# Kernel optimization log

Measured on AMD Instinct MI355X. Metric: run time of the kernel, lower is better.

Reference implementation:

```python
import jax, jax.numpy as jnp
import numpy as np

INPUT_SIZE = 4
HIDDEN = 2048
OUTPUT_SIZE = 2
NOISE_STD = 0.05
ALPHA = 0.2
RANK = 2
N_SUPPORTS = 2
GDIM = 2 * RANK + INPUT_SIZE  # gaussian_basis_dim default
BATCH = 32
SEQ = 1000


def setup_inputs() -> dict:
    key = jax.random.key(0)
    ks = jax.random.split(key, 8)
    inp = jax.random.normal(ks[0], (BATCH, SEQ, INPUT_SIZE), dtype=jnp.float32)
    noise = jax.random.normal(ks[1], (BATCH, SEQ, HIDDEN), dtype=jnp.float32)
    gaussian_basis = jax.random.normal(ks[2], (GDIM, HIDDEN), dtype=jnp.float32)
    # supports: block indicator masks over hidden units (equal split, weights=None)
    sup = np.zeros((N_SUPPORTS, HIDDEN), dtype=np.float32)
    l = HIDDEN // N_SUPPORTS
    for i in range(N_SUPPORTS):
        sup[i, l * i:l * (i + 1)] = 1.0
    supports = jnp.asarray(sup)
    wi_weights = jax.random.normal(ks[3], (INPUT_SIZE, N_SUPPORTS, GDIM), dtype=jnp.float32)
    m_weights = jax.random.normal(ks[4], (RANK, N_SUPPORTS, GDIM), dtype=jnp.float32) / jnp.sqrt(jnp.float32(HIDDEN))
    n_weights = jax.random.normal(ks[5], (RANK, N_SUPPORTS, GDIM), dtype=jnp.float32) / jnp.sqrt(jnp.float32(HIDDEN))
    wo_weights = jax.random.normal(ks[6], (OUTPUT_SIZE, N_SUPPORTS, GDIM), dtype=jnp.float32) / jnp.float32(HIDDEN)
    wi_biases = jnp.zeros((INPUT_SIZE, N_SUPPORTS), dtype=jnp.float32)
    m_biases = jnp.zeros((RANK, N_SUPPORTS), dtype=jnp.float32)
    n_biases = jnp.zeros((RANK, N_SUPPORTS), dtype=jnp.float32)
    h0_weights = jnp.zeros((N_SUPPORTS, GDIM), dtype=jnp.float32)
    return {
        "input": inp, "noise": noise,
        "wi_weights": wi_weights, "m_weights": m_weights, "n_weights": n_weights,
        "wo_weights": wo_weights, "wi_biases": wi_biases, "m_biases": m_biases,
        "n_biases": n_biases, "h0_weights": h0_weights,
        "gaussian_basis": gaussian_basis, "supports": supports,
    }


def _proxy_params(wi_weights, m_weights, n_weights, wo_weights,
                  wi_biases, m_biases, n_biases, h0_weights,
                  gaussian_basis, supports):
    # (X, S, G) @ (G, H) -> (X, S, H); mask by supports (S, H); sum over S
    def mix(w):
        return jnp.einsum('xsg,gh->xsh', w, gaussian_basis)
    wi = jnp.sum(mix(wi_weights) * supports, axis=1) + wi_biases @ supports      # (I, H)
    m = (jnp.sum(mix(m_weights) * supports, axis=1) + m_biases @ supports).T     # (H, R)
    n = (jnp.sum(mix(n_weights) * supports, axis=1) + n_biases @ supports).T     # (H, R)
    wo = jnp.sum(mix(wo_weights) * supports, axis=1).T                            # (H, O)
    h0 = jnp.sum((h0_weights @ gaussian_basis) * supports, axis=0)                # (H,)
    return wi, m, n, wo, h0


def reference(input, noise, wi_weights, m_weights, n_weights, wo_weights,
              wi_biases, m_biases, n_biases, h0_weights, gaussian_basis, supports):
    wi, m, n, wo, h0 = _proxy_params(wi_weights, m_weights, n_weights, wo_weights,
                                     wi_biases, m_biases, n_biases, h0_weights,
                                     gaussian_basis, supports)
    B = input.shape[0]
    # Precompute external input projection for all steps: (B, T, H)
    xin = jnp.einsum('bti,ih->bth', input, wi)
    h_init = jnp.broadcast_to(h0, (B, h0.shape[0]))
    r_init = jnp.tanh(h_init)

    noise_T = jnp.swapaxes(noise, 0, 1)  # (T, B, H)
    xin_T = jnp.swapaxes(xin, 0, 1)      # (T, B, H)

    def step(carry, xs):
        h, r = carry
        noise_t, xin_t = xs
        h = h + NOISE_STD * noise_t + ALPHA * (-h + (r @ n) @ m.T + xin_t)
        r = jnp.tanh(h)
        return (h, r), r

    _, rs = jax.lax.scan(step, (h_init, r_init), (noise_T, xin_T))  # rs: (T, B, H)
    output = jnp.einsum('tbh,ho->bto', rs, wo)  # (B, T, O)
    return output
```

## Files before the change

kernel.cpp:

```cpp
#include <hip/hip_runtime.h>

#define BATCH 32
#define SEQT 1000
#define INSZ 4
#define HID 2048
#define NOISE_STD 0.05f
#define ALPHA 0.2f
#define ONE_M_ALPHA (1.0f - ALPHA)

#define NTHREADS 512
#define NWAVES 8
#define EPT 4
#define PF 4

typedef float v2f __attribute__((ext_vector_type(2)));

__device__ __forceinline__ v2f vfma(v2f a, v2f b, v2f c) { return a * b + c; }

template<int CTRL>
__device__ __forceinline__ float dpp_add(float x) {
    int s = __builtin_amdgcn_update_dpp(0, __float_as_int(x), CTRL, 0xF, 0xF, true);
    return x + __int_as_float(s);
}

__device__ __forceinline__ float wave_sum64_to_lane63(float x) {
    x = dpp_add<0x111>(x);
    x = dpp_add<0x112>(x);
    x = dpp_add<0x114>(x);
    x = dpp_add<0x118>(x);
    x = dpp_add<0x142>(x);
    x = dpp_add<0x143>(x);
    return x;
}

__device__ __forceinline__ float sum8_to_lane7(float x) {
    x = dpp_add<0x111>(x);
    x = dpp_add<0x112>(x);
    x = dpp_add<0x114>(x);
    return x;
}

__device__ __forceinline__ float read_lane7(float x) {
    return __int_as_float(__builtin_amdgcn_readlane(__float_as_int(x), 7));
}

__device__ __forceinline__ float fast_tanh(float x) {
    float e = __expf(2.0f * x);
    return 1.0f - 2.0f * __builtin_amdgcn_rcpf(e + 1.0f);
}

#define LDS_BARRIER() __asm__ volatile("s_waitcnt lgkmcnt(0)\ns_barrier" ::: "memory")

__global__ __launch_bounds__(NTHREADS)
void rnn_kernel(const float* __restrict__ input,
                const float* __restrict__ noise,
                const float* __restrict__ wi_w,
                const float* __restrict__ m_w,
                const float* __restrict__ n_w,
                const float* __restrict__ wo_w,
                const float* __restrict__ wi_b,
                const float* __restrict__ m_b,
                const float* __restrict__ n_b,
                const float* __restrict__ h0_w,
                const float* __restrict__ gb,
                const float* __restrict__ sup,
                float* __restrict__ out)
{
    __shared__ float4 sIn4[SEQT];
    __shared__ __align__(16) float4 sRed[2][NWAVES];

    const int b    = blockIdx.x;
    const int tid  = threadIdx.x;
    const int wave = tid >> 6;
    const int lane = tid & 63;

    const float4* inRow4 = reinterpret_cast<const float4*>(input + (size_t)b * SEQT * INSZ);
    for (int i = tid; i < SEQT; i += NTHREADS)
        sIn4[i] = inRow4[i];

    v2f wiA[INSZ][2];
    v2f mA0v[2], mA1v[2], n0v[2], n1v[2], wo0v[2], wo1v[2], hv[2];
    v2f q0 = {0.f, 0.f}, q1 = q0, q2 = q0, q3 = q0;

    #pragma unroll
    for (int e = 0; e < EPT; ++e) {
        const int h = tid * 4 + e;
        const int pi = e >> 1, pc = e & 1;
        float gv[8];
        #pragma unroll
        for (int g = 0; g < 8; ++g) gv[g] = gb[g * HID + h];
        const float s0 = sup[h];
        const float s1 = sup[HID + h];

        auto mix = [&](const float* w) -> float {
            float a0 = 0.f, a1 = 0.f;
            #pragma unroll
            for (int g = 0; g < 8; ++g) { a0 += w[g] * gv[g]; a1 += w[8 + g] * gv[g]; }
            return s0 * a0 + s1 * a1;
        };

        #pragma unroll
        for (int i = 0; i < INSZ; ++i)
            wiA[i][pi][pc] = ALPHA * (mix(wi_w + i * 16) + wi_b[i * 2 + 0] * s0 + wi_b[i * 2 + 1] * s1);
        mA0v[pi][pc] = ALPHA * (mix(m_w)      + m_b[0] * s0 + m_b[1] * s1);
        mA1v[pi][pc] = ALPHA * (mix(m_w + 16) + m_b[2] * s0 + m_b[3] * s1);
        const float n0 = mix(n_w)      + n_b[0] * s0 + n_b[1] * s1;
        const float n1 = mix(n_w + 16) + n_b[2] * s0 + n_b[3] * s1;
        const float w0 = mix(wo_w);
        const float w1 = mix(wo_w + 16);
        n0v[pi][pc] = n0;  n1v[pi][pc] = n1;
        wo0v[pi][pc] = w0; wo1v[pi][pc] = w1;
        {
            float a0 = 0.f, a1 = 0.f;
            #pragma unroll
            for (int g = 0; g < 8; ++g) { a0 += h0_w[g] * gv[g]; a1 += h0_w[8 + g] * gv[g]; }
            const float h0v = s0 * a0 + s1 * a1;
            hv[pi][pc] = h0v;
            const float r = fast_tanh(h0v);
            q0[pc] += r * n0;  q1[pc] += r * n1;
            q2[pc] += r * w0;  q3[pc] += r * w1;
        }
    }

    const float4* nP4 = reinterpret_cast<const float4*>(noise + (size_t)b * SEQT * HID);
    const int rowStride = HID / 4;
    float4 nb0 = nP4[0 * rowStride + tid];
    float4 nb1 = nP4[1 * rowStride + tid];
    float4 nb2 = nP4[2 * rowStride + tid];
    float4 nb3 = nP4[3 * rowStride + tid];

    float* outRow = out + (size_t)b * SEQT * 2;

    __syncthreads();
    float4 inv0 = sIn4[0];
    float4 inv1 = sIn4[1];
    float4 inv2 = sIn4[2];
    float4 inv3 = sIn4[3];

    auto do_step = [&](int t, float4& nbuf, float4& invReg) {
        const int par = t & 1;
        const float p0 = q0.x + q0.y, p1 = q1.x + q1.y;
        const float p2 = q2.x + q2.y, p3 = q3.x + q3.y;
        const float w0 = wave_sum64_to_lane63(p0);
        const float w1 = wave_sum64_to_lane63(p1);
        const float w2 = wave_sum64_to_lane63(p2);
        const float w3 = wave_sum64_to_lane63(p3);
        if (lane == 63) sRed[par][wave] = make_float4(w0, w1, w2, w3);

        LDS_BARRIER();

        const float4 pr = sRed[par][lane & 7];
        const int tpre = (t + PF < SEQT) ? (t + PF) : (SEQT - 1);
        const float4 nv4 = nbuf;
        nbuf = nP4[(size_t)tpre * rowStride + tid];
        const float4 inv = invReg;
        invReg = sIn4[tpre];

        const v2f nlo = {nv4.x, nv4.y}, nhi = {nv4.z, nv4.w};
        v2f acc0 = wiA[0][0] * inv.x;
        v2f acc1 = wiA[0][1] * inv.x;
        acc0 = vfma(wiA[1][0], inv.y, acc0);  acc1 = vfma(wiA[1][1], inv.y, acc1);
        acc0 = vfma(wiA[2][0], inv.z, acc0);  acc1 = vfma(wiA[2][1], inv.z, acc1);
        acc0 = vfma(wiA[3][0], inv.w, acc0);  acc1 = vfma(wiA[3][1], inv.w, acc1);
        acc0 = acc0 + nlo * NOISE_STD;        acc1 = acc1 + nhi * NOISE_STD;
        acc0 = vfma(hv[0], ONE_M_ALPHA, acc0); acc1 = vfma(hv[1], ONE_M_ALPHA, acc1);

        const float y0 = read_lane7(sum8_to_lane7(pr.x));
        const float y1 = read_lane7(sum8_to_lane7(pr.y));

        if (t > 0 && wave == (t & 7)) {
            const float oz = sum8_to_lane7(pr.z);
            const float ow = sum8_to_lane7(pr.w);
            if (lane == 7)
                *reinterpret_cast<float2*>(outRow + (t - 1) * 2) = make_float2(oz, ow);
        }

        v2f h2a = vfma(mA1v[0], y1, acc0);
        v2f h2b = vfma(mA1v[1], y1, acc1);
        h2a = vfma(mA0v[0], y0, h2a);
        h2b = vfma(mA0v[1], y0, h2b);
        hv[0] = h2a; hv[1] = h2b;
        v2f r2a, r2b;
        r2a.x = fast_tanh(h2a.x); r2a.y = fast_tanh(h2a.y);
        r2b.x = fast_tanh(h2b.x); r2b.y = fast_tanh(h2b.y);
        q0 = r2a * n0v[0];  q0 = vfma(r2b, n0v[1], q0);
        q1 = r2a * n1v[0];  q1 = vfma(r2b, n1v[1], q1);
        q2 = r2a * wo0v[0]; q2 = vfma(r2b, wo0v[1], q2);
        q3 = r2a * wo1v[0]; q3 = vfma(r2b, wo1v[1], q3);
    };

    for (int t = 0; t < SEQT; t += PF) {
        do_step(t,     nb0, inv0);
        do_step(t + 1, nb1, inv1);
        do_step(t + 2, nb2, inv2);
        do_step(t + 3, nb3, inv3);
    }

    {
        const float p2 = q2.x + q2.y, p3 = q3.x + q3.y;
        const float w2 = wave_sum64_to_lane63(p2);
        const float w3 = wave_sum64_to_lane63(p3);
        if (lane == 63) sRed[0][wave] = make_float4(w2, w3, 0.f, 0.f);
        LDS_BARRIER();
        if (wave == 0) {
            const float4 pr = sRed[0][lane & 7];
            const float oz = sum8_to_lane7(pr.x);
            const float ow = sum8_to_lane7(pr.y);
            if (lane == 7)
                *reinterpret_cast<float2*>(outRow + (SEQT - 1) * 2) = make_float2(oz, ow);
        }
    }
}

extern "C" void kernel_launch(void* const* d_in, const int* in_sizes, int n_in,
                              void* d_out, int out_size, void* d_ws, size_t ws_size,
                              hipStream_t stream) {
    const float* input = (const float*)d_in[0];
    const float* noise = (const float*)d_in[1];
    const float* wi_w  = (const float*)d_in[2];
    const float* m_w   = (const float*)d_in[3];
    const float* n_w   = (const float*)d_in[4];
    const float* wo_w  = (const float*)d_in[5];
    const float* wi_b  = (const float*)d_in[6];
    const float* m_b   = (const float*)d_in[7];
    const float* n_b   = (const float*)d_in[8];
    const float* h0_w  = (const float*)d_in[9];
    const float* gb    = (const float*)d_in[10];
    const float* sup   = (const float*)d_in[11];
    float* out = (float*)d_out;

    rnn_kernel<<<dim3(BATCH), dim3(NTHREADS), 0, stream>>>(
        input, noise, wi_w, m_w, n_w, wo_w, wi_b, m_b, n_b, h0_w, gb, sup, out);
}
```

Measured before the change: 877.4 us.

## Defer output wave-reductions past barrier and load input directly from global

After: 940.8 us. 7.2% more time.

```diff
diff --git a/kernel.cpp b/kernel.cpp
--- a/kernel.cpp
+++ b/kernel.cpp
@@ -66,17 +66,12 @@
                 const float* __restrict__ sup,
                 float* __restrict__ out)
 {
-    __shared__ float4 sIn4[SEQT];
     __shared__ __align__(16) float4 sRed[2][NWAVES];
 
     const int b    = blockIdx.x;
     const int tid  = threadIdx.x;
     const int wave = tid >> 6;
     const int lane = tid & 63;
-
-    const float4* inRow4 = reinterpret_cast<const float4*>(input + (size_t)b * SEQT * INSZ);
-    for (int i = tid; i < SEQT; i += NTHREADS)
-        sIn4[i] = inRow4[i];
 
     v2f wiA[INSZ][2];
     v2f mA0v[2], mA1v[2], n0v[2], n1v[2], wo0v[2], wo1v[2], hv[2];
@@ -129,32 +124,36 @@
     float4 nb2 = nP4[2 * rowStride + tid];
     float4 nb3 = nP4[3 * rowStride + tid];
 
+    const float4* inRow4 = reinterpret_cast<const float4*>(input + (size_t)b * SEQT * INSZ);
+    float4 inv0 = inRow4[0];
+    float4 inv1 = inRow4[1];
+    float4 inv2 = inRow4[2];
+    float4 inv3 = inRow4[3];
+
     float* outRow = out + (size_t)b * SEQT * 2;
 
-    __syncthreads();
-    float4 inv0 = sIn4[0];
-    float4 inv1 = sIn4[1];
-    float4 inv2 = sIn4[2];
-    float4 inv3 = sIn4[3];
+    float oz = 0.f, ow = 0.f;
 
     auto do_step = [&](int t, float4& nbuf, float4& invReg) {
         const int par = t & 1;
         const float p0 = q0.x + q0.y, p1 = q1.x + q1.y;
-        const float p2 = q2.x + q2.y, p3 = q3.x + q3.y;
         const float w0 = wave_sum64_to_lane63(p0);
         const float w1 = wave_sum64_to_lane63(p1);
-        const float w2 = wave_sum64_to_lane63(p2);
-        const float w3 = wave_sum64_to_lane63(p3);
-        if (lane == 63) sRed[par][wave] = make_float4(w0, w1, w2, w3);
+        if (lane == 63) sRed[par][wave] = make_float4(w0, w1, oz, ow);
 
         LDS_BARRIER();
 
         const float4 pr = sRed[par][lane & 7];
+
+        const float p2 = q2.x + q2.y, p3 = q3.x + q3.y;
+        const float ozn = wave_sum64_to_lane63(p2);
+        const float own = wave_sum64_to_lane63(p3);
+
         const int tpre = (t + PF < SEQT) ? (t + PF) : (SEQT - 1);
         const float4 nv4 = nbuf;
         nbuf = nP4[(size_t)tpre * rowStride + tid];
         const float4 inv = invReg;
-        invReg = sIn4[tpre];
+        invReg = inRow4[tpre];
 
         const v2f nlo = {nv4.x, nv4.y}, nhi = {nv4.z, nv4.w};
         v2f acc0 = wiA[0][0] * inv.x;
@@ -168,12 +167,13 @@
         const float y0 = read_lane7(sum8_to_lane7(pr.x));
         const float y1 = read_lane7(sum8_to_lane7(pr.y));
 
-        if (t > 0 && wave == (t & 7)) {
-            const float oz = sum8_to_lane7(pr.z);
-            const float ow = sum8_to_lane7(pr.w);
+        if (t >= 2 && wave == (t & 7)) {
+            const float o0 = sum8_to_lane7(pr.z);
+            const float o1 = sum8_to_lane7(pr.w);
             if (lane == 7)
-                *reinterpret_cast<float2*>(outRow + (t - 1) * 2) = make_float2(oz, ow);
+                *reinterpret_cast<float2*>(outRow + (t - 2) * 2) = make_float2(o0, o1);
         }
+        oz = ozn; ow = own;
 
         v2f h2a = vfma(mA1v[0], y1, acc0);
         v2f h2b = vfma(mA1v[1], y1, acc1);
@@ -200,14 +200,18 @@
         const float p2 = q2.x + q2.y, p3 = q3.x + q3.y;
         const float w2 = wave_sum64_to_lane63(p2);
         const float w3 = wave_sum64_to_lane63(p3);
-        if (lane == 63) sRed[0][wave] = make_float4(w2, w3, 0.f, 0.f);
+        if (lane == 63) sRed[0][wave] = make_float4(w2, w3, oz, ow);
         LDS_BARRIER();
         if (wave == 0) {
             const float4 pr = sRed[0][lane & 7];
-            const float oz = sum8_to_lane7(pr.x);
-            const float ow = sum8_to_lane7(pr.y);
-            if (lane == 7)
-                *reinterpret_cast<float2*>(outRow + (SEQT - 1) * 2) = make_float2(oz, ow);
+            const float a999 = sum8_to_lane7(pr.x);
+            const float b999 = sum8_to_lane7(pr.y);
+            const float a998 = sum8_to_lane7(pr.z);
+            const float b998 = sum8_to_lane7(pr.w);
+            if (lane == 7) {
+                *reinterpret_cast<float2*>(outRow + 998 * 2) = make_float2(a998, b998);
+                *reinterpret_cast<float2*>(outRow + 999 * 2) = make_float2(a999, b999);
+            }
         }
     }
 }
```
